# Kernel tuning notes

Hardware: AMD Instinct MI355X
Metric: run time of the kernel (lower is better)

## Reference

```python
import jax, jax.numpy as jnp
import numpy as np

NUM_HEADS = 16
KEY_DIM = 64
D_MODEL = NUM_HEADS * KEY_DIM
BATCH = 2
SEQ = 2048


def _rope_tables(seq_len, dim, dtype):
    # matches RotaryPositionalEmbedding: inv_freq = exp(arange(0,dim,2) * (-ln(10000)/dim))
    pos = jnp.arange(seq_len, dtype=dtype)                      # [S]
    inv_freq = jnp.exp(jnp.arange(0, dim, 2, dtype=dtype) * (-np.log(10000.0) / dim))  # [D/2]
    angles = pos[:, None] * inv_freq[None, :]                   # [S, D/2]
    return jnp.sin(angles), jnp.cos(angles)


def _apply_rope(x, sin, cos):
    # x: [B, S, H, D]; sin/cos: [S, D/2] broadcast over batch and heads
    sin = sin[None, :, None, :]
    cos = cos[None, :, None, :]
    x1, x2 = jnp.split(x, 2, axis=-1)
    return jnp.concatenate([cos * x1 - sin * x2, sin * x1 + cos * x2], axis=-1)


def setup_inputs() -> dict:
    key = jax.random.key(0)
    ks = jax.random.split(key, 5)
    s = 1.0 / np.sqrt(D_MODEL)
    return {
        "inputs": jax.random.normal(ks[0], (BATCH, SEQ, D_MODEL), jnp.float32),
        "Wq": jax.random.normal(ks[1], (D_MODEL, D_MODEL), jnp.float32) * s,
        "bq": jnp.zeros((D_MODEL,), jnp.float32),
        "Wk": jax.random.normal(ks[2], (D_MODEL, D_MODEL), jnp.float32) * s,
        "bk": jnp.zeros((D_MODEL,), jnp.float32),
        "Wv": jax.random.normal(ks[3], (D_MODEL, D_MODEL), jnp.float32) * s,
        "bv": jnp.zeros((D_MODEL,), jnp.float32),
        "Wo": jax.random.normal(ks[4], (D_MODEL, D_MODEL), jnp.float32) * s,
        "bo": jnp.zeros((D_MODEL,), jnp.float32),
    }


def reference(inputs, Wq, bq, Wk, bk, Wv, bv, Wo, bo):
    B, S, _ = inputs.shape
    # QKV projections, split into heads: [B, S, H, Dk]
    q = (inputs @ Wq + bq).reshape(B, S, NUM_HEADS, KEY_DIM)
    k = (inputs @ Wk + bk).reshape(B, S, NUM_HEADS, KEY_DIM)
    v = (inputs @ Wv + bv).reshape(B, S, NUM_HEADS, KEY_DIM)
    # rotary embedding on q/k (per-head dim = KEY_DIM)
    sin, cos = _rope_tables(S, KEY_DIM, inputs.dtype)
    q = _apply_rope(q, sin, cos)
    k = _apply_rope(k, sin, cos)
    # attention: [B, H, S, S]
    scores = jnp.einsum("bshd,bthd->bhst", q, k) / jnp.sqrt(
        jnp.asarray(KEY_DIM, inputs.dtype))
    weights = jax.nn.softmax(scores, axis=-1)  # dropout inactive (training=False)
    ctx = jnp.einsum("bhst,bthd->bshd", weights, v).reshape(B, S, D_MODEL)
    return ctx @ Wo + bo
```

## Files before the change

kernel.cpp:

```cpp
#include <hip/hip_runtime.h>
#include <math.h>

#define NH 16
#define KD 64
#define DMODEL 1024
#define BATCH 2
#define SEQ 2048
#define MROWS (BATCH*SEQ)

typedef float f32x4 __attribute__((ext_vector_type(4)));
typedef float f32x16 __attribute__((ext_vector_type(16)));
typedef __bf16 bf16x8 __attribute__((ext_vector_type(8)));

__device__ __forceinline__ unsigned short f2bf(float x) {
    union { float f; unsigned u; } a; a.f = x;
    unsigned r = a.u + 0x7fffu + ((a.u >> 16) & 1u);
    return (unsigned short)(r >> 16);
}
__device__ __forceinline__ unsigned cvt_pk_bf16(float lo, float hi) {
    unsigned r;
    asm("v_cvt_pk_bf16_f32 %0, %1, %2" : "=v"(r) : "v"(lo), "v"(hi));
    return r;
}
__device__ __forceinline__ float exp2_hw(float x) {
    float r;
    asm("v_exp_f32 %0, %1" : "=v"(r) : "v"(x));
    return r;
}

__device__ __forceinline__ void gl2lds16(const void* gsrc, void* ldst) {
    __builtin_amdgcn_global_load_lds(
        (const __attribute__((address_space(1))) void*)gsrc,
        (__attribute__((address_space(3))) void*)ldst, 16, 0, 0);
}

__global__ __launch_bounds__(256) void k_prep(const float* __restrict__ x,
                                              const float* __restrict__ W0,
                                              const float* __restrict__ W1,
                                              const float* __restrict__ W2,
                                              const float* __restrict__ W3,
                                              float* __restrict__ sin_t,
                                              float* __restrict__ cos_t,
                                              unsigned short* __restrict__ xh,
                                              unsigned short* __restrict__ Th) {
    __shared__ float L[64][65];
    const int bid = blockIdx.x;
    const int tid = threadIdx.x;
    if (bid < 256) {
        int idx = bid * 256 + tid;
        int s = idx >> 5, i = idx & 31;
        float invf = expf((float)(2 * i) * (-logf(10000.0f) / (float)KD));
        float ang = (float)s * invf;
        sin_t[idx] = sinf(ang);
        cos_t[idx] = cosf(ang);
        return;
    }
    if (bid < 4352) {
        int idx = (bid - 256) * 256 + tid;
        float4 v = reinterpret_cast<const float4*>(x)[idx];
        ushort4 h;
        h.x = f2bf(v.x); h.y = f2bf(v.y); h.z = f2bf(v.z); h.w = f2bf(v.w);
        reinterpret_cast<ushort4*>(xh)[idx] = h;
        return;
    }
    int r = bid - 4352;
    int z = r >> 8;
    int rr = r & 255;
    const int n0 = (rr & 15) * 64, k0 = (rr >> 4) * 64;
    const float* W = (z == 0) ? W0 : (z == 1) ? W1 : (z == 2) ? W2 : W3;
    const size_t zoff = (size_t)z * DMODEL * DMODEL;
#pragma unroll
    for (int it = 0; it < 4; ++it) {
        int idx = tid + it * 256;
        int rw = idx >> 4;
        int c4 = (idx & 15) * 4;
        float4 v = *reinterpret_cast<const float4*>(&W[(size_t)(k0 + rw) * DMODEL + n0 + c4]);
        L[rw][c4 + 0] = v.x; L[rw][c4 + 1] = v.y; L[rw][c4 + 2] = v.z; L[rw][c4 + 3] = v.w;
    }
    __syncthreads();
    int rn = tid >> 2;
    int ks = (tid & 3) * 16;
#pragma unroll
    for (int g = 0; g < 4; ++g) {
        ushort4 h;
        h.x = f2bf(L[ks + g * 4 + 0][rn]);
        h.y = f2bf(L[ks + g * 4 + 1][rn]);
        h.z = f2bf(L[ks + g * 4 + 2][rn]);
        h.w = f2bf(L[ks + g * 4 + 3][rn]);
        size_t o = zoff + (size_t)(n0 + rn) * DMODEL + k0 + ks + g * 4;
        *reinterpret_cast<ushort4*>(&Th[o]) = h;
    }
}

__global__ __launch_bounds__(256) void k_mgemm_qkv(const unsigned short* __restrict__ Ah_g,
                                                   const unsigned short* __restrict__ Wp,
                                                   const float* __restrict__ bq,
                                                   const float* __restrict__ bk,
                                                   const float* __restrict__ bv,
                                                   unsigned short* __restrict__ qh_,
                                                   unsigned short* __restrict__ kh_,
                                                   unsigned short* __restrict__ vth,
                                                   const float* __restrict__ sin_t,
                                                   const float* __restrict__ cos_t) {
    __shared__ unsigned short Ah[2][128 * 64];
    __shared__ unsigned short Bh[2][3][64 * 64];
    const int tid = threadIdx.x;
    const int lane = tid & 63;
    const int w = tid >> 6;

    int bid = blockIdx.x;
    int wg = (bid & 7) * 64 + (bid >> 3);
    const int m0 = (wg >> 4) * 128;
    const int n0 = (wg & 15) * 64;
    const size_t WE = (size_t)DMODEL * DMODEL;

    size_t a_goff[4]; int a_ldst[4];
#pragma unroll
    for (int it = 0; it < 4; ++it) {
        int off = it * 4096 + w * 1024 + lane * 16;
        int row = off >> 7;
        int pg = (off >> 4) & 7;
        int lg = pg ^ (row & 7);
        a_goff[it] = (size_t)(m0 + row) * DMODEL + lg * 8;
        a_ldst[it] = it * 2048 + w * 512;
    }
    size_t b_goff[2]; int b_ldst[2];
#pragma unroll
    for (int it = 0; it < 2; ++it) {
        int off = it * 4096 + w * 1024 + lane * 16;
        int row = off >> 7;
        int pg = (off >> 4) & 7;
        int lg = pg ^ (row & 7);
        b_goff[it] = (size_t)(n0 + row) * DMODEL + lg * 8;
        b_ldst[it] = it * 2048 + w * 512;
    }

    int aoff[2][2], boff[4][2];
#pragma unroll
    for (int mf = 0; mf < 2; ++mf)
#pragma unroll
        for (int ks = 0; ks < 2; ++ks) {
            int row = w * 32 + mf * 16 + (lane & 15);
            int g = ks * 4 + (lane >> 4);
            aoff[mf][ks] = row * 64 + ((g ^ (row & 7)) * 8);
        }
#pragma unroll
    for (int nf = 0; nf < 4; ++nf)
#pragma unroll
        for (int ks = 0; ks < 2; ++ks) {
            int row = nf * 16 + (lane & 15);
            int g = ks * 4 + (lane >> 4);
            boff[nf][ks] = row * 64 + ((g ^ (row & 7)) * 8);
        }

    f32x4 acc[3][2][4];
#pragma unroll
    for (int z = 0; z < 3; ++z)
#pragma unroll
        for (int mf = 0; mf < 2; ++mf)
#pragma unroll
            for (int nf = 0; nf < 4; ++nf) acc[z][mf][nf] = (f32x4){0.f, 0.f, 0.f, 0.f};

#define STAGEG(BUF, KT) do {                                                  \
        int k0_ = (KT) * 64;                                                  \
        gl2lds16(Ah_g + a_goff[0] + k0_, &Ah[BUF][a_ldst[0]]);                \
        gl2lds16(Ah_g + a_goff[1] + k0_, &Ah[BUF][a_ldst[1]]);                \
        gl2lds16(Ah_g + a_goff[2] + k0_, &Ah[BUF][a_ldst[2]]);                \
        gl2lds16(Ah_g + a_goff[3] + k0_, &Ah[BUF][a_ldst[3]]);                \
        gl2lds16(Wp + 0 * WE + b_goff[0] + k0_, &Bh[BUF][0][b_ldst[0]]);      \
        gl2lds16(Wp + 0 * WE + b_goff[1] + k0_, &Bh[BUF][0][b_ldst[1]]);      \
        gl2lds16(Wp + 1 * WE + b_goff[0] + k0_, &Bh[BUF][1][b_ldst[0]]);      \
        gl2lds16(Wp + 1 * WE + b_goff[1] + k0_, &Bh[BUF][1][b_ldst[1]]);      \
        gl2lds16(Wp + 2 * WE + b_goff[0] + k0_, &Bh[BUF][2][b_ldst[0]]);      \
        gl2lds16(Wp + 2 * WE + b_goff[1] + k0_, &Bh[BUF][2][b_ldst[1]]);      \
    } while (0)

    STAGEG(0, 0);

    for (int kt = 0; kt < 16; ++kt) {
        const int cur = kt & 1;
        asm volatile("s_waitcnt vmcnt(0)" ::: "memory");
        __builtin_amdgcn_s_barrier();
        if (kt < 15) STAGEG(cur ^ 1, kt + 1);
#pragma unroll
        for (int ks = 0; ks < 2; ++ks) {
            bf16x8 ah[2];
#pragma unroll
            for (int mf = 0; mf < 2; ++mf)
                ah[mf] = *reinterpret_cast<const bf16x8*>(&Ah[cur][aoff[mf][ks]]);
#pragma unroll
            for (int z = 0; z < 3; ++z) {
                bf16x8 bh[4];
#pragma unroll
                for (int nf = 0; nf < 4; ++nf)
                    bh[nf] = *reinterpret_cast<const bf16x8*>(&Bh[cur][z][boff[nf][ks]]);
#pragma unroll
                for (int mf = 0; mf < 2; ++mf)
#pragma unroll
                    for (int nf = 0; nf < 4; ++nf)
                        acc[z][mf][nf] = __builtin_amdgcn_mfma_f32_16x16x32_bf16(ah[mf], bh[nf], acc[z][mf][nf], 0, 0, 0);
            }
        }
    }
#undef STAGEG

    const int c = lane & 15;
    const int rq = lane >> 4;
    float bvq[4], bvk[4], bvv[4];
#pragma unroll
    for (int nf = 0; nf < 4; ++nf) {
        bvq[nf] = bq[n0 + nf * 16 + c];
        bvk[nf] = bk[n0 + nf * 16 + c];
        bvv[nf] = bv[n0 + nf * 16 + c];
    }

#pragma unroll
    for (int mf = 0; mf < 2; ++mf) {
        int mbase = m0 + w * 32 + mf * 16 + rq * 4;
#pragma unroll
        for (int z = 0; z < 2; ++z) {
            const float* bb_ = (z == 0) ? bvq : bvk;
            unsigned short* Ohi = (z == 0) ? qh_ : kh_;
#pragma unroll
            for (int r2 = 0; r2 < 4; ++r2) {
                int m = mbase + r2;
                int srow = m & (SEQ - 1);
                float x0 = acc[z][mf][0][r2] + bb_[0];
                float x1 = acc[z][mf][1][r2] + bb_[1];
                float x2 = acc[z][mf][2][r2] + bb_[2];
                float x3 = acc[z][mf][3][r2] + bb_[3];
                float s0 = sin_t[srow * 32 + c],      c0 = cos_t[srow * 32 + c];
                float s1 = sin_t[srow * 32 + 16 + c], c1 = cos_t[srow * 32 + 16 + c];
                float o0 = c0 * x0 - s0 * x2;
                float o2 = s0 * x0 + c0 * x2;
                float o1 = c1 * x1 - s1 * x3;
                float o3 = s1 * x1 + c1 * x3;
                if (z == 0) {
                    const float qs = 0.18033688011112042f;
                    o0 *= qs; o1 *= qs; o2 *= qs; o3 *= qs;
                }
                float ov[4] = { o0, o1, o2, o3 };
                size_t base = (size_t)m * DMODEL + n0 + c;
#pragma unroll
                for (int nf = 0; nf < 4; ++nf)
                    Ohi[base + nf * 16] = f2bf(ov[nf]);
            }
        }
        {
            int bb = mbase >> 11;
            int s = mbase & (SEQ - 1);
            int h = n0 >> 6;
#pragma unroll
            for (int nf = 0; nf < 4; ++nf) {
                ushort4 h4;
                float v0 = acc[2][mf][nf][0] + bvv[nf];
                float v1 = acc[2][mf][nf][1] + bvv[nf];
                float v2 = acc[2][mf][nf][2] + bvv[nf];
                float v3 = acc[2][mf][nf][3] + bvv[nf];
                h4.x = f2bf(v0); h4.y = f2bf(v1); h4.z = f2bf(v2); h4.w = f2bf(v3);
                int d = nf * 16 + c;
                size_t o = ((size_t)((bb * NH + h) * KD + d)) * SEQ + s;
                *reinterpret_cast<ushort4*>(&vth[o]) = h4;
            }
        }
    }
}

__global__ __launch_bounds__(256) void k_mgemm_o(const unsigned short* __restrict__ Ah_g,
                                                 const unsigned short* __restrict__ Bh_g,
                                                 const float* __restrict__ bias,
                                                 float* __restrict__ Cf) {
    __shared__ unsigned short Ah[2][128 * 64];
    __shared__ unsigned short Bh[2][64 * 64];
    const int tid = threadIdx.x;
    const int lane = tid & 63;
    const int w = tid >> 6;

    int bid = blockIdx.x;
    int wg = (bid & 7) * 64 + (bid >> 3);
    const int m0 = (wg >> 4) * 128;
    const int n0 = (wg & 15) * 64;

    size_t a_goff[4]; int a_ldst[4];
#pragma unroll
    for (int it = 0; it < 4; ++it) {
        int off = it * 4096 + w * 1024 + lane * 16;
        int row = off >> 7;
        int pg = (off >> 4) & 7;
        int lg = pg ^ (row & 7);
        a_goff[it] = (size_t)(m0 + row) * DMODEL + lg * 8;
        a_ldst[it] = it * 2048 + w * 512;
    }
    size_t b_goff[2]; int b_ldst[2];
#pragma unroll
    for (int it = 0; it < 2; ++it) {
        int off = it * 4096 + w * 1024 + lane * 16;
        int row = off >> 7;
        int pg = (off >> 4) & 7;
        int lg = pg ^ (row & 7);
        b_goff[it] = (size_t)(n0 + row) * DMODEL + lg * 8;
        b_ldst[it] = it * 2048 + w * 512;
    }

    int aoff[2][2], boff[4][2];
#pragma unroll
    for (int mf = 0; mf < 2; ++mf)
#pragma unroll
        for (int ks = 0; ks < 2; ++ks) {
            int row = w * 32 + mf * 16 + (lane & 15);
            int g = ks * 4 + (lane >> 4);
            aoff[mf][ks] = row * 64 + ((g ^ (row & 7)) * 8);
        }
#pragma unroll
    for (int nf = 0; nf < 4; ++nf)
#pragma unroll
        for (int ks = 0; ks < 2; ++ks) {
            int row = nf * 16 + (lane & 15);
            int g = ks * 4 + (lane >> 4);
            boff[nf][ks] = row * 64 + ((g ^ (row & 7)) * 8);
        }

    f32x4 acc[2][4];
#pragma unroll
    for (int mf = 0; mf < 2; ++mf)
#pragma unroll
        for (int nf = 0; nf < 4; ++nf) acc[mf][nf] = (f32x4){0.f, 0.f, 0.f, 0.f};

#define STAGEG(BUF, KT) do {                                                  \
        int k0_ = (KT) * 64;                                                  \
        gl2lds16(Ah_g + a_goff[0] + k0_, &Ah[BUF][a_ldst[0]]);                \
        gl2lds16(Ah_g + a_goff[1] + k0_, &Ah[BUF][a_ldst[1]]);                \
        gl2lds16(Ah_g + a_goff[2] + k0_, &Ah[BUF][a_ldst[2]]);                \
        gl2lds16(Ah_g + a_goff[3] + k0_, &Ah[BUF][a_ldst[3]]);                \
        gl2lds16(Bh_g + b_goff[0] + k0_, &Bh[BUF][b_ldst[0]]);                \
        gl2lds16(Bh_g + b_goff[1] + k0_, &Bh[BUF][b_ldst[1]]);                \
    } while (0)

    STAGEG(0, 0);

    for (int kt = 0; kt < 16; ++kt) {
        const int cur = kt & 1;
        asm volatile("s_waitcnt vmcnt(0)" ::: "memory");
        __builtin_amdgcn_s_barrier();
        if (kt < 15) STAGEG(cur ^ 1, kt + 1);
#pragma unroll
        for (int ks = 0; ks < 2; ++ks) {
            bf16x8 ah[2], bh[4];
#pragma unroll
            for (int mf = 0; mf < 2; ++mf)
                ah[mf] = *reinterpret_cast<const bf16x8*>(&Ah[cur][aoff[mf][ks]]);
#pragma unroll
            for (int nf = 0; nf < 4; ++nf)
                bh[nf] = *reinterpret_cast<const bf16x8*>(&Bh[cur][boff[nf][ks]]);
#pragma unroll
            for (int mf = 0; mf < 2; ++mf)
#pragma unroll
                for (int nf = 0; nf < 4; ++nf)
                    acc[mf][nf] = __builtin_amdgcn_mfma_f32_16x16x32_bf16(ah[mf], bh[nf], acc[mf][nf], 0, 0, 0);
        }
    }
#undef STAGEG

    const int c = lane & 15;
    const int rq = lane >> 4;
    float bv[4];
#pragma unroll
    for (int nf = 0; nf < 4; ++nf) bv[nf] = bias[n0 + nf * 16 + c];
#pragma unroll
    for (int mf = 0; mf < 2; ++mf) {
        int mbase = m0 + w * 32 + mf * 16 + rq * 4;
#pragma unroll
        for (int nf = 0; nf < 4; ++nf)
#pragma unroll
            for (int r = 0; r < 4; ++r)
                Cf[(size_t)(mbase + r) * DMODEL + n0 + nf * 16 + c] = acc[mf][nf][r] + bv[nf];
    }
}

__global__ __launch_bounds__(256) void k_attn(const unsigned short* __restrict__ qhi,
                                              const unsigned short* __restrict__ khi,
                                              const unsigned short* __restrict__ vthi,
                                              unsigned short* __restrict__ ch) {
    __shared__ unsigned short Kh[2][64 * 64];
    __shared__ unsigned short Vh[3][64 * 64];

    const int tid  = threadIdx.x;
    const int lane = tid & 63;
    const int w    = tid >> 6;

    int bid = blockIdx.x;
    int wg  = (bid & 7) * 64 + (bid >> 3);
    const int qt = wg & 15;
    const int h  = (wg >> 4) & 15;
    const int b  = wg >> 8;
    const int q0 = qt * 128;

    const int l31 = lane & 31;
    const int lh  = lane >> 5;

    bf16x8 qf[4];
#pragma unroll
    for (int ks = 0; ks < 4; ++ks) {
        int row = q0 + w * 32 + l31;
        qf[ks] = *reinterpret_cast<const bf16x8*>(
            qhi + ((size_t)(b * SEQ + row) * NH + h) * KD + ks * 16 + lh * 8);
    }

    size_t gK[2], gV[2]; int ld_[2];
#pragma unroll
    for (int it = 0; it < 2; ++it) {
        int off = it * 4096 + tid * 16;
        int row = off >> 7;
        int pg = (off >> 4) & 7;
        int lg = pg ^ (row & 7);
        gK[it] = ((size_t)(b * SEQ + row) * NH + h) * KD + lg * 8;
        gV[it] = ((size_t)(b * NH + h) * KD + row) * SEQ + lg * 8;
        ld_[it] = it * 2048 + w * 512;
    }

    int foff[2][4];
#pragma unroll
    for (int tb = 0; tb < 2; ++tb)
#pragma unroll
        for (int ks = 0; ks < 4; ++ks)
            foff[tb][ks] = (tb * 32 + l31) * 64 + (((ks * 2 + lh) ^ (lane & 7)) * 8);

    f32x16 acc[2], l_acc;
#pragma unroll
    for (int db = 0; db < 2; ++db)
#pragma unroll
        for (int r = 0; r < 16; ++r) acc[db][r] = 0.f;
#pragma unroll
    for (int r = 0; r < 16; ++r) l_acc[r] = 0.f;

    unsigned paw[4][4];
    union U8 { unsigned u[4]; bf16x8 v; };
    U8 ones;
    ones.u[0] = 0x3F803F80u; ones.u[1] = 0x3F803F80u;
    ones.u[2] = 0x3F803F80u; ones.u[3] = 0x3F803F80u;

#define STAGE(KB, VB, TT) do {                                               \
        size_t kadv = (size_t)(TT) * 64 * NH * KD;                           \
        size_t vadv = (size_t)(TT) * 64;                                     \
        gl2lds16(khi  + gK[0] + kadv, &Kh[KB][ld_[0]]);                      \
        gl2lds16(khi  + gK[1] + kadv, &Kh[KB][ld_[1]]);                      \
        gl2lds16(vthi + gV[0] + vadv, &Vh[VB][ld_[0]]);                      \
        gl2lds16(vthi + gV[1] + vadv, &Vh[VB][ld_[1]]);                      \
    } while (0)

#define PV_STEP(VSRC) do {                                                   \
        _Pragma("unroll")                                                    \
        for (int ks = 0; ks < 4; ++ks) {                                     \
            U8 pa; pa.u[0] = paw[ks][0]; pa.u[1] = paw[ks][1];               \
            pa.u[2] = paw[ks][2]; pa.u[3] = paw[ks][3];                      \
            _Pragma("unroll")                                                \
            for (int db = 0; db < 2; ++db) {                                 \
                bf16x8 vf = *reinterpret_cast<const bf16x8*>(&Vh[VSRC][foff[db][ks]]); \
                acc[db] = __builtin_amdgcn_mfma_f32_32x32x16_bf16(pa.v, vf, acc[db], 0, 0, 0); \
            }                                                                \
            l_acc = __builtin_amdgcn_mfma_f32_32x32x16_bf16(pa.v, ones.v, l_acc, 0, 0, 0); \
        }                                                                    \
    } while (0)

    STAGE(0, 0, 0);

    int vnext = 1;
    int vprev = 2;

    for (int t = 0; t < 32; ++t) {
        const int ck = t & 1;
        asm volatile("s_waitcnt vmcnt(0)" ::: "memory");
        __builtin_amdgcn_s_barrier();
        if (t < 31) STAGE(ck ^ 1, vnext, t + 1);

        __builtin_amdgcn_s_setprio(1);
        f32x16 s[2];
#pragma unroll
        for (int tb = 0; tb < 2; ++tb) {
#pragma unroll
            for (int r = 0; r < 16; ++r) s[tb][r] = 0.f;
#pragma unroll
            for (int ks = 0; ks < 4; ++ks) {
                bf16x8 kf = *reinterpret_cast<const bf16x8*>(&Kh[ck][foff[tb][ks]]);
                s[tb] = __builtin_amdgcn_mfma_f32_32x32x16_bf16(kf, qf[ks], s[tb], 0, 0, 0);
            }
        }
        if (t > 0) PV_STEP(vprev);
        __builtin_amdgcn_s_setprio(0);

#pragma unroll
        for (int tb = 0; tb < 2; ++tb) {
            float e[16];
#pragma unroll
            for (int r = 0; r < 16; ++r)
                e[r] = exp2_hw(s[tb][r]);
#pragma unroll
            for (int half = 0; half < 2; ++half) {
                unsigned pk01 = cvt_pk_bf16(e[half * 8 + 0], e[half * 8 + 1]);
                unsigned pk23 = cvt_pk_bf16(e[half * 8 + 2], e[half * 8 + 3]);
                unsigned pk45 = cvt_pk_bf16(e[half * 8 + 4], e[half * 8 + 5]);
                unsigned pk67 = cvt_pk_bf16(e[half * 8 + 6], e[half * 8 + 7]);
                asm volatile("v_permlane32_swap_b32 %0, %1" : "+v"(pk01), "+v"(pk45));
                asm volatile("v_permlane32_swap_b32 %0, %1" : "+v"(pk23), "+v"(pk67));
                paw[tb * 2 + half][0] = pk01;
                paw[tb * 2 + half][1] = pk23;
                paw[tb * 2 + half][2] = pk45;
                paw[tb * 2 + half][3] = pk67;
            }
        }

        vnext = (vnext == 2) ? 0 : vnext + 1;
        vprev = (vprev == 2) ? 0 : vprev + 1;
    }

    PV_STEP(vprev);
#undef PV_STEP
#undef STAGE

#pragma unroll
    for (int db = 0; db < 2; ++db) {
#pragma unroll
        for (int r = 0; r < 16; ++r) {
            int q = (r & 3) + 8 * (r >> 2) + 4 * lh;
            int qg = q0 + w * 32 + q;
            int d = db * 32 + l31;
            ch[((size_t)(b * SEQ + qg) * NH + h) * KD + d] = f2bf(acc[db][r] / l_acc[r]);
        }
    }
}

extern "C" void kernel_launch(void* const* d_in, const int* in_sizes, int n_in,
                              void* d_out, int out_size, void* d_ws, size_t ws_size,
                              hipStream_t stream) {
    const float* x  = (const float*)d_in[0];
    const float* Wq = (const float*)d_in[1];
    const float* bq = (const float*)d_in[2];
    const float* Wk = (const float*)d_in[3];
    const float* bk = (const float*)d_in[4];
    const float* Wv = (const float*)d_in[5];
    const float* bv = (const float*)d_in[6];
    const float* Wo = (const float*)d_in[7];
    const float* bo = (const float*)d_in[8];
    float* out = (float*)d_out;

    const size_t NE = (size_t)MROWS * DMODEL;
    const size_t WE = (size_t)DMODEL * DMODEL;
    float* ws    = (float*)d_ws;
    float* sin_t = ws;
    float* cos_t = sin_t + SEQ * 32;
    unsigned short* p = (unsigned short*)(cos_t + SEQ * 32);
    unsigned short* xh   = p; p += NE;
    unsigned short* qh_  = p; p += NE;
    unsigned short* kh_  = p; p += NE;
    unsigned short* vth  = p; p += NE;
    unsigned short* wth  = p; p += 4 * WE;
    unsigned short* ctxh = xh;

    k_prep<<<5376, 256, 0, stream>>>(x, Wq, Wk, Wv, Wo, sin_t, cos_t, xh, wth);

    k_mgemm_qkv<<<512, 256, 0, stream>>>(xh, wth, bq, bk, bv, qh_, kh_, vth, sin_t, cos_t);

    k_attn<<<512, 256, 0, stream>>>(qh_, kh_, vth, ctxh);

    k_mgemm_o<<<512, 256, 0, stream>>>(ctxh, wth + 3 * WE, bo, out);
}
```

Before: 109.9 us.

## Process two KV tiles per barrier in attention loop with doubled LDS staging

Restructures the attention main loop to stage and consume two 64-key tiles per iteration, halving the number of vmcnt waits and workgroup barriers. The QK MFMA of each sub-tile is interleaved with the PV MFMA of the previous sub-tile, and the exp/pack step runs between them. This doubles the LDS footprint for K and V buffers, which can lower the number of resident workgroups per CU. An unused dead macro is also left in.

```diff
diff --git a/kernel.cpp b/kernel.cpp
--- a/kernel.cpp
+++ b/kernel.cpp
@@ -381,8 +381,8 @@
                                               const unsigned short* __restrict__ khi,
                                               const unsigned short* __restrict__ vthi,
                                               unsigned short* __restrict__ ch) {
-    __shared__ unsigned short Kh[2][64 * 64];
-    __shared__ unsigned short Vh[3][64 * 64];
+    __shared__ unsigned short Kh[2][2][64 * 64];
+    __shared__ unsigned short Vh[3][2][64 * 64];
 
     const int tid  = threadIdx.x;
     const int lane = tid & 63;
@@ -439,39 +439,76 @@
     ones.u[0] = 0x3F803F80u; ones.u[1] = 0x3F803F80u;
     ones.u[2] = 0x3F803F80u; ones.u[3] = 0x3F803F80u;
 
-#define STAGE(KB, VB, TT) do {                                               \
+#define STAGE1(KB, VB, TI, TT) do {                                          \
         size_t kadv = (size_t)(TT) * 64 * NH * KD;                           \
         size_t vadv = (size_t)(TT) * 64;                                     \
-        gl2lds16(khi  + gK[0] + kadv, &Kh[KB][ld_[0]]);                      \
-        gl2lds16(khi  + gK[1] + kadv, &Kh[KB][ld_[1]]);                      \
-        gl2lds16(vthi + gV[0] + vadv, &Vh[VB][ld_[0]]);                      \
-        gl2lds16(vthi + gV[1] + vadv, &Vh[VB][ld_[1]]);                      \
+        gl2lds16(khi  + gK[0] + kadv, &Kh[KB][TI][ld_[0]]);                  \
+        gl2lds16(khi  + gK[1] + kadv, &Kh[KB][TI][ld_[1]]);                  \
+        gl2lds16(vthi + gV[0] + vadv, &Vh[VB][TI][ld_[0]]);                  \
+        gl2lds16(vthi + gV[1] + vadv, &Vh[VB][TI][ld_[1]]);                  \
     } while (0)
 
-#define PV_STEP(VSRC) do {                                                   \
+#define QK_STEP(SREG, KB, TI) do {                                           \
+        _Pragma("unroll")                                                    \
+        for (int r = 0; r < 16; ++r) SREG[r] = 0.f;                          \
+        _Pragma("unroll")                                                    \
+        for (int ks = 0; ks < 4; ++ks) {                                     \
+            bf16x8 kf = *reinterpret_cast<const bf16x8*>(&Kh[KB][TI][foff[0][ks] & 4095]); \
+            (void)kf;                                                        \
+        }                                                                    \
+    } while (0)
+#undef QK_STEP
+
+#define PV_STEP(VB, TI) do {                                                 \
         _Pragma("unroll")                                                    \
         for (int ks = 0; ks < 4; ++ks) {                                     \
             U8 pa; pa.u[0] = paw[ks][0]; pa.u[1] = paw[ks][1];               \
             pa.u[2] = paw[ks][2]; pa.u[3] = paw[ks][3];                      \
             _Pragma("unroll")                                                \
             for (int db = 0; db < 2; ++db) {                                 \
-                bf16x8 vf = *reinterpret_cast<const bf16x8*>(&Vh[VSRC][foff[db][ks]]); \
+                bf16x8 vf = *reinterpret_cast<const bf16x8*>(&Vh[VB][TI][foff[db][ks]]); \
                 acc[db] = __builtin_amdgcn_mfma_f32_32x32x16_bf16(pa.v, vf, acc[db], 0, 0, 0); \
             }                                                                \
             l_acc = __builtin_amdgcn_mfma_f32_32x32x16_bf16(pa.v, ones.v, l_acc, 0, 0, 0); \
         }                                                                    \
     } while (0)
 
-    STAGE(0, 0, 0);
-
-    int vnext = 1;
-    int vprev = 2;
-
-    for (int t = 0; t < 32; ++t) {
-        const int ck = t & 1;
+#define EXP_PACK(SREGS) do {                                                 \
+        _Pragma("unroll")                                                    \
+        for (int tb = 0; tb < 2; ++tb) {                                     \
+            float e[16];                                                     \
+            _Pragma("unroll")                                                \
+            for (int r = 0; r < 16; ++r) e[r] = exp2_hw(SREGS[tb][r]);       \
+            _Pragma("unroll")                                                \
+            for (int half = 0; half < 2; ++half) {                           \
+                unsigned pk01 = cvt_pk_bf16(e[half * 8 + 0], e[half * 8 + 1]); \
+                unsigned pk23 = cvt_pk_bf16(e[half * 8 + 2], e[half * 8 + 3]); \
+                unsigned pk45 = cvt_pk_bf16(e[half * 8 + 4], e[half * 8 + 5]); \
+                unsigned pk67 = cvt_pk_bf16(e[half * 8 + 6], e[half * 8 + 7]); \
+                asm volatile("v_permlane32_swap_b32 %0, %1" : "+v"(pk01), "+v"(pk45)); \
+                asm volatile("v_permlane32_swap_b32 %0, %1" : "+v"(pk23), "+v"(pk67)); \
+                paw[tb * 2 + half][0] = pk01;                                \
+                paw[tb * 2 + half][1] = pk23;                                \
+                paw[tb * 2 + half][2] = pk45;                                \
+                paw[tb * 2 + half][3] = pk67;                                \
+            }                                                                \
+        }                                                                    \
+    } while (0)
+
+    STAGE1(0, 0, 0, 0);
+    STAGE1(0, 0, 1, 1);
+
+    for (int p = 0; p < 16; ++p) {
+        const int pb   = p & 1;
+        const int vb   = p % 3;
+        const int vbm1 = (p + 2) % 3;
         asm volatile("s_waitcnt vmcnt(0)" ::: "memory");
         __builtin_amdgcn_s_barrier();
-        if (t < 31) STAGE(ck ^ 1, vnext, t + 1);
+        if (p < 15) {
+            const int vn = (p + 1) % 3;
+            STAGE1(pb ^ 1, vn, 0, 2 * p + 2);
+            STAGE1(pb ^ 1, vn, 1, 2 * p + 3);
+        }
 
         __builtin_amdgcn_s_setprio(1);
         f32x16 s[2];
@@ -481,41 +518,35 @@
             for (int r = 0; r < 16; ++r) s[tb][r] = 0.f;
 #pragma unroll
             for (int ks = 0; ks < 4; ++ks) {
-                bf16x8 kf = *reinterpret_cast<const bf16x8*>(&Kh[ck][foff[tb][ks]]);
+                bf16x8 kf = *reinterpret_cast<const bf16x8*>(&Kh[pb][0][foff[tb][ks]]);
                 s[tb] = __builtin_amdgcn_mfma_f32_32x32x16_bf16(kf, qf[ks], s[tb], 0, 0, 0);
             }
         }
-        if (t > 0) PV_STEP(vprev);
+        if (p > 0) PV_STEP(vbm1, 1);
         __builtin_amdgcn_s_setprio(0);
-
+        EXP_PACK(s);
+
+        __builtin_amdgcn_s_setprio(1);
+        f32x16 s2[2];
 #pragma unroll
         for (int tb = 0; tb < 2; ++tb) {
-            float e[16];
-#pragma unroll
-            for (int r = 0; r < 16; ++r)
-                e[r] = exp2_hw(s[tb][r]);
-#pragma unroll
-            for (int half = 0; half < 2; ++half) {
-                unsigned pk01 = cvt_pk_bf16(e[half * 8 + 0], e[half * 8 + 1]);
-                unsigned pk23 = cvt_pk_bf16(e[half * 8 + 2], e[half * 8 + 3]);
-                unsigned pk45 = cvt_pk_bf16(e[half * 8 + 4], e[half * 8 + 5]);
-                unsigned pk67 = cvt_pk_bf16(e[half * 8 + 6], e[half * 8 + 7]);
-                asm volatile("v_permlane32_swap_b32 %0, %1" : "+v"(pk01), "+v"(pk45));
-                asm volatile("v_permlane32_swap_b32 %0, %1" : "+v"(pk23), "+v"(pk67));
-                paw[tb * 2 + half][0] = pk01;
-                paw[tb * 2 + half][1] = pk23;
-                paw[tb * 2 + half][2] = pk45;
-                paw[tb * 2 + half][3] = pk67;
+#pragma unroll
+            for (int r = 0; r < 16; ++r) s2[tb][r] = 0.f;
+#pragma unroll
+            for (int ks = 0; ks < 4; ++ks) {
+                bf16x8 kf = *reinterpret_cast<const bf16x8*>(&Kh[pb][1][foff[tb][ks]]);
+                s2[tb] = __builtin_amdgcn_mfma_f32_32x32x16_bf16(kf, qf[ks], s2[tb], 0, 0, 0);
             }
         }
-
-        vnext = (vnext == 2) ? 0 : vnext + 1;
-        vprev = (vprev == 2) ? 0 : vprev + 1;
-    }
-
-    PV_STEP(vprev);
+        PV_STEP(vb, 0);
+        __builtin_amdgcn_s_setprio(0);
+        EXP_PACK(s2);
+    }
+
+    PV_STEP(0, 1);
 #undef PV_STEP
-#undef STAGE
+#undef EXP_PACK
+#undef STAGE1
 
 #pragma unroll
     for (int db = 0; db < 2; ++db) {
```

After: 110.5 us. No clear change (+0.6%).
